# Kernel tuning notes

Hardware: AMD Instinct MI355X
Metric: run time of the kernel (lower is better)

The kernel has to match this reference:

```python
import jax, jax.numpy as jnp
import numpy as np

N, E, H, XD, ED, YD, L = 10000, 640000, 128, 8, 8, 112, 4
EPS_MSG = 1e-7   # GENConv message eps
EPS_SM = 1e-16   # pyg softmax denom eps
EPS_LN = 1e-5    # layernorm eps


def node_ln(x, g, b):
    # torch.nn.LayerNorm over last dim
    m = x.mean(axis=-1, keepdims=True)
    v = x.var(axis=-1, keepdims=True)
    return (x - m) * jax.lax.rsqrt(v + EPS_LN) * g + b


def graph_ln(x, g, b):
    # pyg LayerNorm mode='graph' (no batch): global mean/std over all nodes+channels
    xc = x - x.mean()
    std = jnp.sqrt((xc * xc).mean())
    return xc / (std + EPS_LN) * g + b


def setup_inputs() -> dict:
    key = jax.random.key(0)
    ks = jax.random.split(key, 10)
    rn = lambda k, s, sc: jax.random.normal(k, s, jnp.float32) * sc
    return {
        "x": jax.random.normal(ks[0], (N, XD), jnp.float32),
        "edge_index": jax.random.randint(ks[1], (2, E), 0, N),
        "edge_attr": jax.random.normal(ks[2], (E, ED), jnp.float32),
        "Wn": rn(ks[3], (XD, H), 0.3), "bn": jnp.zeros((H,), jnp.float32),
        "We": rn(ks[4], (ED, H), 0.3), "be": jnp.zeros((H,), jnp.float32),
        "t": jnp.ones((L,), jnp.float32),
        "W1": rn(ks[5], (L, H, 2 * H), 0.08), "b1": jnp.zeros((L, 2 * H), jnp.float32),
        "g1": jnp.ones((L, 2 * H), jnp.float32), "bt1": jnp.zeros((L, 2 * H), jnp.float32),
        "W2": rn(ks[6], (L, 2 * H, H), 0.08), "b2": jnp.zeros((L, H), jnp.float32),
        "lng": jnp.ones((L, H), jnp.float32), "lnb": jnp.zeros((L, H), jnp.float32),
        "Wout": rn(ks[7], (H, YD), 0.08), "bout": jnp.zeros((YD,), jnp.float32),
    }


def reference(x, edge_index, edge_attr, Wn, bn, We, be, t, W1, b1, g1, bt1,
              W2, b2, lng, lnb, Wout, bout):
    src, dst = edge_index[0], edge_index[1]
    h = x @ Wn + bn                       # [N,H] node encoder
    ea = edge_attr @ We + be              # [E,H] edge encoder

    def gen_conv(h, i):
        msg = jax.nn.relu(h[src] + ea) + EPS_MSG          # [E,H]
        logit = msg * t[i]
        mx = jax.ops.segment_max(logit, dst, num_segments=N)
        ex = jnp.exp(logit - mx[dst])
        den = jax.ops.segment_sum(ex, dst, num_segments=N)
        alpha = ex / (den[dst] + EPS_SM)
        agg = jax.ops.segment_sum(alpha * msg, dst, num_segments=N) + h  # root add
        z = jax.nn.relu(graph_ln(agg @ W1[i] + b1[i], g1[i], bt1[i]))
        return z @ W2[i] + b2[i]

    h = gen_conv(h, 0)                    # first layer: conv only
    for i in range(1, L):                 # res+ blocks (dropout off: eval)
        r = jax.nn.relu(node_ln(h, lng[i], lnb[i]))
        h = h + gen_conv(r, i)
    h = jax.nn.relu(node_ln(h, lng[0], lnb[0]))  # layers[0].act(layers[0].norm(x))
    return h @ Wout + bout
```

## Files before the change

kernel.cpp:

```cpp
#include <hip/hip_runtime.h>
#include <math.h>

#define NN 10000
#define NE 640000
#define H 128
#define H2 256
#define XD 8
#define ED 8
#define YD 112
#define NL 4
#define EPS_MSG 1e-7f
#define EPS_SM 1e-16f
#define EPS_LN 1e-5f
#define TM 8
#define NB1 (NN / TM)
#define TNO 16
#define NBO (NN / TNO)

typedef _Float16 h2 __attribute__((ext_vector_type(2)));

__global__ void hist_k(const int* __restrict__ dst, int* __restrict__ counts) {
    int e = blockIdx.x * 256 + threadIdx.x;
    if (e < NE) atomicAdd(&counts[dst[e]], 1);
}

__global__ void scan_k(const int* __restrict__ counts, int* __restrict__ rowptr) {
    __shared__ int part[1024];
    int tid = threadIdx.x;
    const int CH = (NN + 1023) / 1024;
    int base = tid * CH;
    int s = 0;
    for (int j = 0; j < CH; j++) { int i = base + j; if (i < NN) s += counts[i]; }
    part[tid] = s; __syncthreads();
    for (int off = 1; off < 1024; off <<= 1) {
        int v = (tid >= off) ? part[tid - off] : 0;
        __syncthreads();
        part[tid] += v;
        __syncthreads();
    }
    int run = part[tid] - s;
    for (int j = 0; j < CH; j++) {
        int i = base + j;
        if (i < NN) { rowptr[i] = run; run += counts[i]; }
    }
    if (tid == 1023) rowptr[NN] = run;
}

__global__ void scatter_k(const int* __restrict__ dst, const int* __restrict__ rowptr,
                          int* __restrict__ fill, int* __restrict__ perm) {
    int e = blockIdx.x * 256 + threadIdx.x;
    if (e >= NE) return;
    int d = dst[e];
    int pos = rowptr[d] + atomicAdd(&fill[d], 1);
    perm[pos] = e;
}

__global__ void __launch_bounds__(256) packenc_k(
    const int* __restrict__ perm, const int* __restrict__ src,
    const float* __restrict__ eattr, int* __restrict__ srcs,
    _Float16* __restrict__ eacsr,
    const float* __restrict__ x, const float* __restrict__ Wn,
    const float* __restrict__ bn, float* __restrict__ h,
    _Float16* __restrict__ rh16) {
    int b = blockIdx.x;
    if (b < 2500) {
        int pos = b * 256 + threadIdx.x;
        int e = perm[pos];
        srcs[pos] = src[e];
        const float4* ein = (const float4*)eattr;
        float4 a = ein[(size_t)e * 2];
        float4 bb = ein[(size_t)e * 2 + 1];
        float4 pk;
        _Float16* pp = (_Float16*)&pk;
        pp[0] = (_Float16)a.x; pp[1] = (_Float16)a.y; pp[2] = (_Float16)a.z; pp[3] = (_Float16)a.w;
        pp[4] = (_Float16)bb.x; pp[5] = (_Float16)bb.y; pp[6] = (_Float16)bb.z; pp[7] = (_Float16)bb.w;
        ((float4*)eacsr)[pos] = pk;
    } else {
        int bb = b - 2500;
        int c = threadIdx.x & 127, ln = threadIdx.x >> 7;
        int n = bb * 2 + ln;
        const float4* xr = (const float4*)(x + (size_t)n * XD);
        float4 x0 = xr[0], x1 = xr[1];
        float acc = bn[c];
        acc = fmaf(x0.x, Wn[0 * H + c], acc); acc = fmaf(x0.y, Wn[1 * H + c], acc);
        acc = fmaf(x0.z, Wn[2 * H + c], acc); acc = fmaf(x0.w, Wn[3 * H + c], acc);
        acc = fmaf(x1.x, Wn[4 * H + c], acc); acc = fmaf(x1.y, Wn[5 * H + c], acc);
        acc = fmaf(x1.z, Wn[6 * H + c], acc); acc = fmaf(x1.w, Wn[7 * H + c], acc);
        h[(size_t)n * H + c] = acc;
        rh16[(size_t)n * H + c] = (_Float16)acc;
    }
}

__global__ void __launch_bounds__(512) ea_mm1_k(
    const float* __restrict__ rin, const _Float16* __restrict__ rh16,
    const int* __restrict__ rowptr,
    const int* __restrict__ srcs, const _Float16* __restrict__ eacsr,
    const float* __restrict__ We, const float* __restrict__ be,
    const float* __restrict__ tptr, int layer,
    const float* __restrict__ W1i, const float* __restrict__ b1i,
    float* __restrict__ y1, float* __restrict__ part) {
    int nb = blockIdx.x, tid = threadIdx.x;
    int n0 = nb * TM;
    __shared__ float a[TM][H];

    {
        int wv = tid >> 6, l = tid & 63;
        int c0 = 2 * l;
        int n = n0 + wv;
        h2 wA[4], wB[4];
#pragma unroll
        for (int k = 0; k < 4; k++) {
            wA[k][0] = (_Float16)We[(2 * k) * H + c0];
            wA[k][1] = (_Float16)We[(2 * k + 1) * H + c0];
            wB[k][0] = (_Float16)We[(2 * k) * H + c0 + 1];
            wB[k][1] = (_Float16)We[(2 * k + 1) * H + c0 + 1];
        }
        float becA = be[c0], becB = be[c0 + 1];
        float ts2 = tptr[layer] * 1.44269504088896f;
        int beg = __builtin_amdgcn_readfirstlane(rowptr[n]);
        int end = __builtin_amdgcn_readfirstlane(rowptr[n + 1]);
        const float2 rv = *(const float2*)(rin + (size_t)n * H + c0);
        float denA = 0.f, numA = 0.f, denB = 0.f, numB = 0.f;
#pragma unroll 4
        for (int j = beg; j < end; ++j) {
            int sn = srcs[j];
            float4 raw = *(const float4*)(eacsr + (size_t)j * ED);
            const h2* ep = (const h2*)&raw;
            h2 hv2 = *(const h2*)(rh16 + (size_t)sn * H + c0);
            float hvA = (float)hv2[0], hvB = (float)hv2[1];
            float pA = __builtin_amdgcn_fdot2(ep[0], wA[0], becA, false);
            pA = __builtin_amdgcn_fdot2(ep[1], wA[1], pA, false);
            pA = __builtin_amdgcn_fdot2(ep[2], wA[2], pA, false);
            pA = __builtin_amdgcn_fdot2(ep[3], wA[3], pA, false);
            float pB = __builtin_amdgcn_fdot2(ep[0], wB[0], becB, false);
            pB = __builtin_amdgcn_fdot2(ep[1], wB[1], pB, false);
            pB = __builtin_amdgcn_fdot2(ep[2], wB[2], pB, false);
            pB = __builtin_amdgcn_fdot2(ep[3], wB[3], pB, false);
            float msgA = fmaxf(hvA + pA, 0.f) + EPS_MSG;
            float msgB = fmaxf(hvB + pB, 0.f) + EPS_MSG;
            float peA = __builtin_amdgcn_exp2f(msgA * ts2);
            float peB = __builtin_amdgcn_exp2f(msgB * ts2);
            denA += peA; numA = fmaf(peA, msgA, numA);
            denB += peB; numB = fmaf(peB, msgB, numB);
        }
        float2 av;
        av.x = numA / (denA + EPS_SM) + rv.x;
        av.y = numB / (denB + EPS_SM) + rv.y;
        *(float2*)&a[wv][c0] = av;
    }
    __syncthreads();

    int o = tid & 255, half = tid >> 8;
    int rb = half * 4;
    float acc[4];
#pragma unroll
    for (int i = 0; i < 4; i++) acc[i] = 0.f;
    for (int k = 0; k < H; k += 4) {
        float w0 = W1i[k * H2 + o];
        float w1 = W1i[(k + 1) * H2 + o];
        float w2 = W1i[(k + 2) * H2 + o];
        float w3 = W1i[(k + 3) * H2 + o];
#pragma unroll
        for (int i = 0; i < 4; i++) {
            float4 av = *(const float4*)&a[rb + i][k];
            acc[i] = fmaf(av.x, w0, acc[i]);
            acc[i] = fmaf(av.y, w1, acc[i]);
            acc[i] = fmaf(av.z, w2, acc[i]);
            acc[i] = fmaf(av.w, w3, acc[i]);
        }
    }
    float bo = b1i[o];
    float ps = 0.f, ps2 = 0.f;
#pragma unroll
    for (int i = 0; i < 4; i++) {
        float v = acc[i] + bo;
        y1[(size_t)(n0 + rb + i) * H2 + o] = v;
        ps += v; ps2 += v * v;
    }
#pragma unroll
    for (int off = 32; off; off >>= 1) { ps += __shfl_xor(ps, off); ps2 += __shfl_xor(ps2, off); }
    __shared__ float red[16];
    int w8 = tid >> 6;
    if ((tid & 63) == 0) { red[w8] = ps; red[8 + w8] = ps2; }
    __syncthreads();
    if (tid == 0) {
        float S = 0.f, S2 = 0.f;
#pragma unroll
        for (int i = 0; i < 8; i++) { S += red[i]; S2 += red[8 + i]; }
        part[nb * 2] = S;
        part[nb * 2 + 1] = S2;
    }
}

__global__ void __launch_bounds__(256) mm2_k(const float* __restrict__ y1,
    const float* __restrict__ g1i, const float* __restrict__ bt1i,
    const float* __restrict__ W2i, const float* __restrict__ b2i,
    const float* __restrict__ part, float* __restrict__ h,
    const float* __restrict__ lgp, const float* __restrict__ lbp,
    float* __restrict__ r, _Float16* __restrict__ rh16, int first) {
    int nb = blockIdx.x, tid = threadIdx.x;
    int o = tid & 127, half = tid >> 7;
    int rb = half * 4;
    int n0 = nb * TM;
    float s = 0.f, s2 = 0.f;
    for (int i = tid; i < NB1; i += 256) { s += part[2 * i]; s2 += part[2 * i + 1]; }
#pragma unroll
    for (int off = 32; off; off >>= 1) { s += __shfl_xor(s, off); s2 += __shfl_xor(s2, off); }
    __shared__ float sred[8];
    int w4 = tid >> 6;
    if ((tid & 63) == 0) { sred[w4] = s; sred[4 + w4] = s2; }
    __syncthreads();
    const float M = (float)NN * (float)H2;
    float m = (sred[0] + sred[1] + sred[2] + sred[3]) / M;
    float var = fmaxf((sred[4] + sred[5] + sred[6] + sred[7]) / M - m * m, 0.f);
    float istd = 1.f / (sqrtf(var) + EPS_LN);

    __shared__ float z[TM][H2];
    __syncthreads();
    {
        const float4* y4 = (const float4*)(y1 + (size_t)n0 * H2);
        const float4* g4 = (const float4*)g1i;
        const float4* b4 = (const float4*)bt1i;
        float4* z4 = (float4*)z;
#pragma unroll
        for (int t = tid; t < TM * H2 / 4; t += 256) {
            int k4 = t & 63;
            float4 v = y4[t];
            float4 g = g4[k4], b = b4[k4];
            v.x = fmaxf((v.x - m) * istd * g.x + b.x, 0.f);
            v.y = fmaxf((v.y - m) * istd * g.y + b.y, 0.f);
            v.z = fmaxf((v.z - m) * istd * g.z + b.z, 0.f);
            v.w = fmaxf((v.w - m) * istd * g.w + b.w, 0.f);
            z4[t] = v;
        }
    }
    __syncthreads();
    float acc[4];
#pragma unroll
    for (int i = 0; i < 4; i++) acc[i] = 0.f;
    for (int k = 0; k < H2; k += 4) {
        float w0 = W2i[k * H + o];
        float w1 = W2i[(k + 1) * H + o];
        float w2 = W2i[(k + 2) * H + o];
        float w3 = W2i[(k + 3) * H + o];
#pragma unroll
        for (int i = 0; i < 4; i++) {
            float4 zv = *(const float4*)&z[rb + i][k];
            acc[i] = fmaf(zv.x, w0, acc[i]);
            acc[i] = fmaf(zv.y, w1, acc[i]);
            acc[i] = fmaf(zv.z, w2, acc[i]);
            acc[i] = fmaf(zv.w, w3, acc[i]);
        }
    }
    float bo = b2i[o];
    float vv[4];
#pragma unroll
    for (int i = 0; i < 4; i++) {
        size_t idx = (size_t)(n0 + rb + i) * H + o;
        float v = acc[i] + bo;
        if (!first) v += h[idx];
        h[idx] = v;
        vv[i] = v;
    }
    __shared__ float rs[2][2][4], rs2[2][2][4];
    int w2i_ = (tid >> 6) & 1;
#pragma unroll
    for (int i = 0; i < 4; i++) {
        float ss = vv[i], ss2 = vv[i] * vv[i];
#pragma unroll
        for (int off = 32; off; off >>= 1) { ss += __shfl_xor(ss, off); ss2 += __shfl_xor(ss2, off); }
        if ((tid & 63) == 0) { rs[half][w2i_][i] = ss; rs2[half][w2i_][i] = ss2; }
    }
    __syncthreads();
    float gc = lgp[o], bc = lbp[o];
#pragma unroll
    for (int i = 0; i < 4; i++) {
        float S = rs[half][0][i] + rs[half][1][i];
        float S2 = rs2[half][0][i] + rs2[half][1][i];
        float mn = S * (1.f / H);
        float vr = S2 * (1.f / H) - mn * mn;
        float inv = rsqrtf(vr + EPS_LN);
        float ov = fmaxf((vv[i] - mn) * inv * gc + bc, 0.f);
        size_t idx = (size_t)(n0 + rb + i) * H + o;
        r[idx] = ov;
        rh16[idx] = (_Float16)ov;
    }
}

__global__ void __launch_bounds__(128) mmout_k(const float* __restrict__ r,
    const float* __restrict__ Wout, const float* __restrict__ bout,
    float* __restrict__ out) {
    int nb = blockIdx.x, o = threadIdx.x;
    int n0 = nb * TNO;
    __shared__ float a[TNO][H];
    {
        const float4* r4 = (const float4*)(r + (size_t)n0 * H);
        float4* a4 = (float4*)a;
        for (int t = o; t < TNO * H / 4; t += 128) a4[t] = r4[t];
    }
    __syncthreads();
    if (o < YD) {
        float acc[TNO];
#pragma unroll
        for (int i = 0; i < TNO; i++) acc[i] = 0.f;
        for (int k = 0; k < H; k += 4) {
            float w0 = Wout[k * YD + o];
            float w1 = Wout[(k + 1) * YD + o];
            float w2 = Wout[(k + 2) * YD + o];
            float w3 = Wout[(k + 3) * YD + o];
#pragma unroll
            for (int i = 0; i < TNO; i++) {
                float4 av = *(const float4*)&a[i][k];
                acc[i] = fmaf(av.x, w0, acc[i]);
                acc[i] = fmaf(av.y, w1, acc[i]);
                acc[i] = fmaf(av.z, w2, acc[i]);
                acc[i] = fmaf(av.w, w3, acc[i]);
            }
        }
        float bo = bout[o];
#pragma unroll
        for (int i = 0; i < TNO; i++) out[(size_t)(n0 + i) * YD + o] = acc[i] + bo;
    }
}

extern "C" void kernel_launch(void* const* d_in, const int* in_sizes, int n_in,
                              void* d_out, int out_size, void* d_ws, size_t ws_size,
                              hipStream_t stream) {
    const float* x    = (const float*)d_in[0];
    const int*   ei   = (const int*)d_in[1];
    const float* eattr= (const float*)d_in[2];
    const float* Wn   = (const float*)d_in[3];
    const float* bn   = (const float*)d_in[4];
    const float* We   = (const float*)d_in[5];
    const float* be   = (const float*)d_in[6];
    const float* t    = (const float*)d_in[7];
    const float* W1   = (const float*)d_in[8];
    const float* b1   = (const float*)d_in[9];
    const float* g1   = (const float*)d_in[10];
    const float* bt1  = (const float*)d_in[11];
    const float* W2   = (const float*)d_in[12];
    const float* b2   = (const float*)d_in[13];
    const float* lng  = (const float*)d_in[14];
    const float* lnb  = (const float*)d_in[15];
    const float* Wout = (const float*)d_in[16];
    const float* bout = (const float*)d_in[17];
    float* out = (float*)d_out;

    const int* src = ei;
    const int* dst = ei + NE;

    char* ws = (char*)d_ws;
    size_t off = 0;
    auto alloc = [&](size_t bytes) -> char* {
        char* p = ws + off;
        off += (bytes + 255) & ~(size_t)255;
        return p;
    };
    int*      counts = (int*)alloc((size_t)NN * 2 * 4);
    int*      fill   = counts + NN;
    int*      rowptr = (int*)alloc((size_t)(NN + 1) * 4);
    int*      perm   = (int*)alloc((size_t)NE * 4);
    int*      srcs   = (int*)alloc((size_t)NE * 4);
    _Float16* eacsr  = (_Float16*)alloc((size_t)NE * ED * 2);
    float*    h      = (float*)alloc((size_t)NN * H * 4);
    float*    r      = (float*)alloc((size_t)NN * H * 4);
    _Float16* rh16   = (_Float16*)alloc((size_t)NN * H * 2);
    float*    y1     = (float*)alloc((size_t)NN * H2 * 4);
    float*    part   = (float*)alloc((size_t)NB1 * 2 * 4);
    (void)ws_size; (void)in_sizes; (void)n_in; (void)out_size;

    hipMemsetAsync(counts, 0, (size_t)NN * 2 * 4, stream);

    hist_k<<<(NE + 255) / 256, 256, 0, stream>>>(dst, counts);
    scan_k<<<1, 1024, 0, stream>>>(counts, rowptr);
    scatter_k<<<(NE + 255) / 256, 256, 0, stream>>>(dst, rowptr, fill, perm);
    packenc_k<<<2500 + NN / 2, 256, 0, stream>>>(perm, src, eattr, srcs, eacsr,
                                                 x, Wn, bn, h, rh16);

    for (int i = 0; i < NL; i++) {
        const float* cin = (i == 0) ? h : r;
        ea_mm1_k<<<NB1, 512, 0, stream>>>(cin, rh16, rowptr, srcs, eacsr, We, be, t, i,
                                          W1 + (size_t)i * H * H2, b1 + i * H2, y1, part);
        int nx = (i == NL - 1) ? 0 : (i + 1);
        mm2_k<<<NB1, 256, 0, stream>>>(y1, g1 + i * H2, bt1 + i * H2,
                                       W2 + (size_t)i * H2 * H, b2 + i * H, part, h,
                                       lng + nx * H, lnb + nx * H, r, rh16, (i == 0) ? 1 : 0);
    }
    mmout_k<<<NBO, 128, 0, stream>>>(r, Wout, bout, out);
}
```

Measured before the change: 473.9 us.

## Split each node's edge loop across two waves and halve rows per block

```diff
diff --git a/kernel.cpp b/kernel.cpp
--- a/kernel.cpp
+++ b/kernel.cpp
@@ -12,6 +12,8 @@
 #define EPS_MSG 1e-7f
 #define EPS_SM 1e-16f
 #define EPS_LN 1e-5f
+#define TMA 4
+#define NBA (NN / TMA)
 #define TM 8
 #define NB1 (NN / TM)
 #define TNO 16
@@ -49,7 +51,6 @@
 __global__ void scatter_k(const int* __restrict__ dst, const int* __restrict__ rowptr,
                           int* __restrict__ fill, int* __restrict__ perm) {
     int e = blockIdx.x * 256 + threadIdx.x;
-    if (e >= NE) return;
     int d = dst[e];
     int pos = rowptr[d] + atomicAdd(&fill[d], 1);
     perm[pos] = e;
@@ -100,13 +101,16 @@
     const float* __restrict__ W1i, const float* __restrict__ b1i,
     float* __restrict__ y1, float* __restrict__ part) {
     int nb = blockIdx.x, tid = threadIdx.x;
-    int n0 = nb * TM;
-    __shared__ float a[TM][H];
+    int n0 = nb * TMA;
+    __shared__ float denp[2][TMA][H];
+    __shared__ float nump[2][TMA][H];
+    __shared__ float a[TMA][H];
 
     {
         int wv = tid >> 6, l = tid & 63;
+        int nd = wv >> 1, p = wv & 1;
         int c0 = 2 * l;
-        int n = n0 + wv;
+        int n = n0 + nd;
         h2 wA[4], wB[4];
 #pragma unroll
         for (int k = 0; k < 4; k++) {
@@ -119,10 +123,9 @@
         float ts2 = tptr[layer] * 1.44269504088896f;
         int beg = __builtin_amdgcn_readfirstlane(rowptr[n]);
         int end = __builtin_amdgcn_readfirstlane(rowptr[n + 1]);
-        const float2 rv = *(const float2*)(rin + (size_t)n * H + c0);
         float denA = 0.f, numA = 0.f, denB = 0.f, numB = 0.f;
 #pragma unroll 4
-        for (int j = beg; j < end; ++j) {
+        for (int j = beg + p; j < end; j += 2) {
             int sn = srcs[j];
             float4 raw = *(const float4*)(eacsr + (size_t)j * ED);
             const h2* ep = (const h2*)&raw;
@@ -143,25 +146,28 @@
             denA += peA; numA = fmaf(peA, msgA, numA);
             denB += peB; numB = fmaf(peB, msgB, numB);
         }
-        float2 av;
-        av.x = numA / (denA + EPS_SM) + rv.x;
-        av.y = numB / (denB + EPS_SM) + rv.y;
-        *(float2*)&a[wv][c0] = av;
+        denp[p][nd][c0] = denA; denp[p][nd][c0 + 1] = denB;
+        nump[p][nd][c0] = numA; nump[p][nd][c0 + 1] = numB;
+    }
+    __syncthreads();
+    {
+        int nd = tid >> 7, c = tid & 127;
+        float den = denp[0][nd][c] + denp[1][nd][c];
+        float num = nump[0][nd][c] + nump[1][nd][c];
+        a[nd][c] = num / (den + EPS_SM) + rin[(size_t)(n0 + nd) * H + c];
     }
     __syncthreads();
 
     int o = tid & 255, half = tid >> 8;
-    int rb = half * 4;
-    float acc[4];
-#pragma unroll
-    for (int i = 0; i < 4; i++) acc[i] = 0.f;
+    int rb = half * 2;
+    float acc[2] = {0.f, 0.f};
     for (int k = 0; k < H; k += 4) {
         float w0 = W1i[k * H2 + o];
         float w1 = W1i[(k + 1) * H2 + o];
         float w2 = W1i[(k + 2) * H2 + o];
         float w3 = W1i[(k + 3) * H2 + o];
 #pragma unroll
-        for (int i = 0; i < 4; i++) {
+        for (int i = 0; i < 2; i++) {
             float4 av = *(const float4*)&a[rb + i][k];
             acc[i] = fmaf(av.x, w0, acc[i]);
             acc[i] = fmaf(av.y, w1, acc[i]);
@@ -172,7 +178,7 @@
     float bo = b1i[o];
     float ps = 0.f, ps2 = 0.f;
 #pragma unroll
-    for (int i = 0; i < 4; i++) {
+    for (int i = 0; i < 2; i++) {
         float v = acc[i] + bo;
         y1[(size_t)(n0 + rb + i) * H2 + o] = v;
         ps += v; ps2 += v * v;
@@ -203,7 +209,7 @@
     int rb = half * 4;
     int n0 = nb * TM;
     float s = 0.f, s2 = 0.f;
-    for (int i = tid; i < NB1; i += 256) { s += part[2 * i]; s2 += part[2 * i + 1]; }
+    for (int i = tid; i < NBA; i += 256) { s += part[2 * i]; s2 += part[2 * i + 1]; }
 #pragma unroll
     for (int off = 32; off; off >>= 1) { s += __shfl_xor(s, off); s2 += __shfl_xor(s2, off); }
     __shared__ float sred[8];
@@ -366,20 +372,21 @@
     float*    r      = (float*)alloc((size_t)NN * H * 4);
     _Float16* rh16   = (_Float16*)alloc((size_t)NN * H * 2);
     float*    y1     = (float*)alloc((size_t)NN * H2 * 4);
-    float*    part   = (float*)alloc((size_t)NB1 * 2 * 4);
+    float*    part   = (float*)alloc((size_t)NBA * 2 * 4);
     (void)ws_size; (void)in_sizes; (void)n_in; (void)out_size;
 
     hipMemsetAsync(counts, 0, (size_t)NN * 2 * 4, stream);
 
     hist_k<<<(NE + 255) / 256, 256, 0, stream>>>(dst, counts);
     scan_k<<<1, 1024, 0, stream>>>(counts, rowptr);
-    scatter_k<<<(NE + 255) / 256, 256, 0, stream>>>(dst, rowptr, fill, perm);
+    scatter_k<<<NE / 256, 256, 0, stream>>>(dst, rowptr, fill, perm);
     packenc_k<<<2500 + NN / 2, 256, 0, stream>>>(perm, src, eattr, srcs, eacsr,
                                                  x, Wn, bn, h, rh16);
 
     for (int i = 0; i < NL; i++) {
         const float* cin = (i == 0) ? h : r;
-        ea_mm1_k<<<NB1, 512, 0, stream>>>(cin, rh16, rowptr, srcs, eacsr, We, be, t, i,
+        ea_mm1_k<<<NBA, 512, 0, stream>>>(cin, rh16, rowptr, srcs, eacsr,
+                                          We, be, t, i,
                                           W1 + (size_t)i * H * H2, b1 + i * H2, y1, part);
         int nx = (i == NL - 1) ? 0 : (i + 1);
         mm2_k<<<NB1, 256, 0, stream>>>(y1, g1 + i * H2, bt1 + i * H2,
```

After: 524.6 us. 10.7% more time.
